# Performance work log

Hardware: AMD Instinct MI355X
Metric: run time of the kernel (lower is better)

## Reference

```python
import jax, jax.numpy as jnp
import numpy as np

N = 25600            # 64 graphs x 400 ROIs
F_IN = 400
H = 128
E = 512000           # 8000 edges per graph
B = 64
G = 8
OUT = 2
NPG = 400            # nodes per graph
EPG = E // B         # edges per graph
BN_EPS = 1e-5


def _xavier(k, shape):
    lim = float(np.sqrt(6.0 / (shape[0] + shape[1])))
    return jax.random.uniform(k, shape, jnp.float32, -lim, lim)


def setup_inputs() -> dict:
    key = jax.random.key(0)
    ks = jax.random.split(key, 16)
    inp = {}
    inp["x"] = jax.random.normal(ks[0], (N, F_IN), jnp.float32)
    # within-graph random edges: local index + graph offset
    src_l = jax.random.randint(ks[1], (E,), 0, NPG, jnp.int32)
    dst_l = jax.random.randint(ks[2], (E,), 0, NPG, jnp.int32)
    off = (jnp.arange(E, dtype=jnp.int32) // EPG) * NPG
    inp["edge_index"] = jnp.stack([src_l + off, dst_l + off])
    inp["batch"] = (jnp.arange(N, dtype=jnp.int32) // NPG)
    inp["group_ids"] = jax.random.randint(ks[3], (N,), 0, G, jnp.int32)
    inp["ge"] = _xavier(ks[4], (G, 2))
    inp["he"] = _xavier(ks[5], (2, 2))
    dims = [(F_IN + 4, H), (H, H), (H, H)]
    for i, (di, do) in enumerate(dims):
        k1, k2 = jax.random.split(ks[6 + i])
        inp[f"w{i}a"] = _xavier(k1, (di, do))
        inp[f"b{i}a"] = jnp.zeros((do,), jnp.float32)
        inp[f"g{i}"] = jnp.ones((do,), jnp.float32)
        inp[f"be{i}"] = jnp.zeros((do,), jnp.float32)
        inp[f"w{i}b"] = _xavier(k2, (do, do))
        inp[f"b{i}b"] = jnp.zeros((do,), jnp.float32)
    inp["wfa"] = _xavier(ks[10], (H, H))
    inp["bfa"] = jnp.zeros((H,), jnp.float32)
    inp["wfb"] = _xavier(ks[11], (H, OUT))
    inp["bfb"] = jnp.zeros((OUT,), jnp.float32)
    return inp


def _bn(h, gamma, beta):
    # BatchNorm1d in training mode: stats over node dimension
    mu = jnp.mean(h, axis=0, keepdims=True)
    var = jnp.var(h, axis=0, keepdims=True)
    return gamma * (h - mu) * jax.lax.rsqrt(var + BN_EPS) + beta


def reference(x, edge_index, batch, group_ids, ge, he,
              w0a, b0a, g0, be0, w0b, b0b,
              w1a, b1a, g1, be1, w1b, b1b,
              w2a, b2a, g2, be2, w2b, b2b,
              wfa, bfa, wfb, bfb):
    n = x.shape[0]
    hemi = jnp.arange(n) % 2                      # [1::2] = 1
    h = jnp.concatenate([x, ge[group_ids], he[hemi]], axis=-1)  # [N, F_IN+4]
    src, dst = edge_index[0], edge_index[1]
    layers = [(w0a, b0a, g0, be0, w0b, b0b),
              (w1a, b1a, g1, be1, w1b, b1b),
              (w2a, b2a, g2, be2, w2b, b2b)]
    for wa, ba, g, be, wb, bb in layers:
        # GINConv (eps=0): x_i + sum_{(j,i)} x_j, then 2-layer MLP w/ batchnorm
        agg = jax.ops.segment_sum(h[src], dst, num_segments=N)
        z = h + agg
        z = jax.nn.relu(_bn(z @ wa + ba, g, be))  # dropout = identity (eval)
        h = jax.nn.relu(z @ wb + bb)              # outer ReLU from forward()
    pooled = jax.ops.segment_sum(h, batch, num_segments=B)  # global_add_pool
    return jax.nn.relu(pooled @ wfa + bfa) @ wfb + bfb
```

## Files before the change

kernel.cpp:

```cpp
#include <hip/hip_runtime.h>

#define N_NODES 25600
#define F_IN 400
#define NE 512000
#define NB 64
#define NPG 400
#define EPG 8000
#define BN_EPS 1e-5f

#define S_ROWS 448
#define S_COLS 448
#define AGG_TILES 14
#define SB_RPB 112
#define K0PAD 448

typedef __attribute__((ext_vector_type(8))) short short8;
typedef __attribute__((ext_vector_type(4))) short short4_t;
typedef __attribute__((ext_vector_type(4))) float floatx4;

__device__ __forceinline__ unsigned short f2bf(float f) {
    unsigned int u = __float_as_uint(f);
    u += 0x7FFF + ((u >> 16) & 1);
    return (unsigned short)(u >> 16);
}
__device__ __forceinline__ float bf2f(unsigned short s) {
    return __uint_as_float((unsigned int)s << 16);
}
__device__ __forceinline__ short u8bf(unsigned v) {
    return (short)(__float_as_uint((float)v) >> 16);
}


__global__ __launch_bounds__(256) void prep(const int* __restrict__ src,
                                            const int* __restrict__ dst,
                                            unsigned char* __restrict__ Sb,
                                            const float* __restrict__ wa0, const float* __restrict__ wa1,
                                            const float* __restrict__ wa2, const float* __restrict__ wb0,
                                            const float* __restrict__ wb1, const float* __restrict__ wb2,
                                            unsigned short* __restrict__ t0, unsigned short* __restrict__ t1,
                                            unsigned short* __restrict__ t2, unsigned short* __restrict__ t3,
                                            unsigned short* __restrict__ t4, unsigned short* __restrict__ t5,
                                            float* __restrict__ pstat) {
    __shared__ int cnt32[SB_RPB * NPG / 4];
    int tid = threadIdx.x;
    if (blockIdx.x < 256) {
        int b = blockIdx.x;
        int g = b >> 2, part = b & 3;
        int r0 = part * SB_RPB;
        for (int i = tid; i < SB_RPB * NPG / 4; i += 256) cnt32[i] = 0;
        __syncthreads();
        int ebase = g * EPG, nbase = g * NPG;
        for (int e = tid; e < EPG; e += 256) {
            int d = dst[ebase + e] - nbase;
            int dr = d - r0;
            if ((unsigned)dr < (unsigned)SB_RPB) {
                int s = src[ebase + e] - nbase;
                int idx = dr * NPG + s;
                atomicAdd(&cnt32[idx >> 2], (int)(1u << ((idx & 3) * 8)));
            }
        }
        __syncthreads();
        const unsigned char* cb = (const unsigned char*)cnt32;
        for (int i = tid; i < SB_RPB * (S_COLS / 8); i += 256) {
            int rr = i / (S_COLS / 8), c8 = (i % (S_COLS / 8)) * 8;
            int R = r0 + rr;
            unsigned lo = 0, hi = 0;
#pragma unroll
            for (int j = 0; j < 4; ++j) {
                int c = c8 + j;
                unsigned v = 0;
                if (R < NPG && c < NPG) v = (unsigned)cb[rr * NPG + c] + (c == R ? 1u : 0u);
                lo |= v << (8 * j);
            }
#pragma unroll
            for (int j = 0; j < 4; ++j) {
                int c = c8 + 4 + j;
                unsigned v = 0;
                if (R < NPG && c < NPG) v = (unsigned)cb[rr * NPG + c] + (c == R ? 1u : 0u);
                hi |= v << (8 * j);
            }
            uint2 o = {lo, hi};
            *(uint2*)&Sb[((size_t)g * S_ROWS + R) * S_COLS + c8] = o;
        }
        return;
    }
    int idx = (blockIdx.x - 256) * 256 + tid;
    if (idx < 3 * 2048) pstat[idx] = 0.f;
    if (idx < 128 * K0PAD) {
        int n = idx / K0PAD, k = idx - n * K0PAD;
        t0[idx] = (k < 400) ? f2bf(wa0[(size_t)k * 128 + n]) : (unsigned short)0;
        return;
    }
    idx -= 128 * K0PAD;
    if (idx >= 5 * 128 * 128) return;
    int seg = idx >> 14;
    int r = idx & 16383;
    int n = r >> 7, k = r & 127;
    const float* srcs[5] = {wb0, wa1, wb1, wa2, wb2};
    unsigned short* dsts[5] = {t3, t1, t4, t2, t5};
    dsts[seg][r] = f2bf(srcs[seg][(size_t)k * 128 + n]);
}


__global__ __launch_bounds__(256) void gemm_embed32(const float* __restrict__ A,
                                                    const unsigned short* __restrict__ Wt,
                                                    const float* __restrict__ Wfull,
                                                    const int* __restrict__ gid,
                                                    const float* __restrict__ ge,
                                                    const float* __restrict__ he,
                                                    unsigned short* __restrict__ CtT) {
    __shared__ __align__(16) unsigned short As[32][72];
    __shared__ __align__(16) unsigned short Bs[128][72];
    __shared__ float Wex[4][128];
    int tid = threadIdx.x;
    int m0 = blockIdx.x * 32;
    int wave = tid >> 6, lane = tid & 63;
    int wcol = wave * 32;
    int fm = lane & 15, quad = lane >> 4;

    for (int i = tid; i < 512; i += 256)
        Wex[i >> 7][i & 127] = Wfull[(size_t)(400 + (i >> 7)) * 128 + (i & 127)];

    floatx4 acc[2][2];
#pragma unroll
    for (int rt = 0; rt < 2; ++rt)
#pragma unroll
        for (int ct = 0; ct < 2; ++ct) acc[rt][ct] = (floatx4){0.f, 0.f, 0.f, 0.f};

    const int rA = tid >> 3, kcA = (tid & 7) * 8;
    const int nB = tid >> 1, kcB = (tid & 1) * 32;
    float4 aP0, aP1;
    short8 bP0, bP1, bP2, bP3;

    auto loadK = [&](int ks) {
        int k0 = ks * 64;
        int kg = k0 + kcA;
        if (kg + 7 < 400) {
            const float* ar = A + (size_t)(m0 + rA) * F_IN + kg;
            aP0 = *(const float4*)ar;
            aP1 = *(const float4*)(ar + 4);
        } else {
            const float* ar = A + (size_t)(m0 + rA) * F_IN;
            float v[8];
#pragma unroll
            for (int j = 0; j < 8; ++j) v[j] = (kg + j < 400) ? ar[kg + j] : 0.f;
            aP0 = (float4){v[0], v[1], v[2], v[3]};
            aP1 = (float4){v[4], v[5], v[6], v[7]};
        }
        const unsigned short* wr = Wt + (size_t)nB * K0PAD + k0 + kcB;
        bP0 = *(const short8*)wr;
        bP1 = *(const short8*)(wr + 8);
        bP2 = *(const short8*)(wr + 16);
        bP3 = *(const short8*)(wr + 24);
    };

    loadK(0);
    for (int ks = 0; ks < 7; ++ks) {
        {
            short8 s;
            s[0] = (short)f2bf(aP0.x); s[1] = (short)f2bf(aP0.y);
            s[2] = (short)f2bf(aP0.z); s[3] = (short)f2bf(aP0.w);
            s[4] = (short)f2bf(aP1.x); s[5] = (short)f2bf(aP1.y);
            s[6] = (short)f2bf(aP1.z); s[7] = (short)f2bf(aP1.w);
            *(short8*)&As[rA][kcA] = s;
            *(short8*)&Bs[nB][kcB] = bP0;
            *(short8*)&Bs[nB][kcB + 8] = bP1;
            *(short8*)&Bs[nB][kcB + 16] = bP2;
            *(short8*)&Bs[nB][kcB + 24] = bP3;
        }
        __syncthreads();
        if (ks + 1 < 7) loadK(ks + 1);
#pragma unroll
        for (int k0l = 0; k0l < 64; k0l += 32) {
            short8 af[2], bf[2];
            af[0] = *(const short8*)&As[fm][k0l + quad * 8];
            af[1] = *(const short8*)&As[16 + fm][k0l + quad * 8];
#pragma unroll
            for (int ct = 0; ct < 2; ++ct)
                bf[ct] = *(const short8*)&Bs[wcol + ct * 16 + fm][k0l + quad * 8];
#pragma unroll
            for (int rt = 0; rt < 2; ++rt)
#pragma unroll
                for (int ct = 0; ct < 2; ++ct)
                    acc[rt][ct] = __builtin_amdgcn_mfma_f32_16x16x32_bf16(
                        af[rt], bf[ct], acc[rt][ct], 0, 0, 0);
        }
        __syncthreads();
    }

#pragma unroll
    for (int rt = 0; rt < 2; ++rt) {
#pragma unroll
        for (int ct = 0; ct < 2; ++ct) {
            int col = wcol + ct * 16 + fm;
            int row0 = m0 + rt * 16 + quad * 4;
            ushort4 o;
#pragma unroll
            for (int r = 0; r < 4; ++r) {
                int row = row0 + r;
                int gv = gid[row];
                float v = acc[rt][ct][r]
                        + ge[gv * 2] * Wex[0][col] + ge[gv * 2 + 1] * Wex[1][col]
                        + he[(row & 1) * 2] * Wex[2][col] + he[(row & 1) * 2 + 1] * Wex[3][col];
                ((unsigned short*)&o)[r] = f2bf(v);
            }
            *(ushort4*)&CtT[(size_t)col * N_NODES + row0] = o;
        }
    }
}


__global__ __launch_bounds__(256) void agg_mfma(const unsigned char* __restrict__ Sb,
                                                const unsigned short* __restrict__ tT,
                                                const float* __restrict__ bias,
                                                unsigned short* __restrict__ z,
                                                float* __restrict__ psumG,
                                                float* __restrict__ psqG) {
    __shared__ __align__(16) unsigned short As[32][72];
    __shared__ __align__(16) unsigned short Bs[128][72];
    __shared__ float sw[4][2][16], qw[4][2][16];
    int tid = threadIdx.x;
    int b = blockIdx.x;
    int g = b & 63;
    int tile = b >> 6;
    int m0l = tile * 32;
    int node0 = g * NPG;
    int wave = tid >> 6, lane = tid & 63;
    int wcol = wave * 32;
    int fm = lane & 15, quad = lane >> 4;

    floatx4 acc[2][2];
#pragma unroll
    for (int rt = 0; rt < 2; ++rt)
#pragma unroll
        for (int ct = 0; ct < 2; ++ct) acc[rt][ct] = (floatx4){0.f, 0.f, 0.f, 0.f};

    const int rA = tid >> 3, kcA = (tid & 7) * 8;
    const int nB = tid >> 1, kcB = (tid & 1) * 32;
    uint2 aP;
    short8 bP0, bP1, bP2, bP3;

    auto loadK = [&](int ks) {
        int k0 = ks * 64;
        aP = *(const uint2*)(Sb + ((size_t)g * S_ROWS + m0l + rA) * S_COLS + k0 + kcA);
        const unsigned short* p = tT + (size_t)nB * N_NODES + node0 + k0 + kcB;
        bP0 = *(const short8*)p;
        bP1 = *(const short8*)(p + 8);
        bP2 = *(const short8*)(p + 16);
        bP3 = *(const short8*)(p + 24);
    };

    loadK(0);
    for (int ks = 0; ks < S_COLS / 64; ++ks) {
        {
            short8 s;
#pragma unroll
            for (int j = 0; j < 4; ++j) s[j] = u8bf((aP.x >> (8 * j)) & 255u);
#pragma unroll
            for (int j = 0; j < 4; ++j) s[4 + j] = u8bf((aP.y >> (8 * j)) & 255u);
            *(short8*)&As[rA][kcA] = s;
            *(short8*)&Bs[nB][kcB] = bP0;
            *(short8*)&Bs[nB][kcB + 8] = bP1;
            *(short8*)&Bs[nB][kcB + 16] = bP2;
            *(short8*)&Bs[nB][kcB + 24] = bP3;
        }
        __syncthreads();
        if (ks + 1 < S_COLS / 64) loadK(ks + 1);
#pragma unroll
        for (int k0l = 0; k0l < 64; k0l += 32) {
            short8 af[2], bf[2];
            af[0] = *(const short8*)&As[fm][k0l + quad * 8];
            af[1] = *(const short8*)&As[16 + fm][k0l + quad * 8];
#pragma unroll
            for (int ct = 0; ct < 2; ++ct)
                bf[ct] = *(const short8*)&Bs[wcol + ct * 16 + fm][k0l + quad * 8];
#pragma unroll
            for (int rt = 0; rt < 2; ++rt)
#pragma unroll
                for (int ct = 0; ct < 2; ++ct)
                    acc[rt][ct] = __builtin_amdgcn_mfma_f32_16x16x32_bf16(
                        af[rt], bf[ct], acc[rt][ct], 0, 0, 0);
        }
        __syncthreads();
    }

    {
        float scol[2] = {0.f, 0.f}, qcol[2] = {0.f, 0.f};
#pragma unroll
        for (int rt = 0; rt < 2; ++rt) {
#pragma unroll
            for (int ct = 0; ct < 2; ++ct) {
                int col = wcol + ct * 16 + fm;
                float bv = bias[col];
                int rbase = m0l + rt * 16 + quad * 4;
#pragma unroll
                for (int r = 0; r < 4; ++r) {
                    int rloc = rbase + r;
                    if (rloc < NPG) {
                        float v = acc[rt][ct][r] + bv;
                        z[(size_t)(node0 + rloc) * 128 + col] = f2bf(v);
                        scol[ct] += v;
                        qcol[ct] += v * v;
                    }
                }
            }
        }
#pragma unroll
        for (int ct = 0; ct < 2; ++ct) {
            scol[ct] += __shfl_xor(scol[ct], 16);
            scol[ct] += __shfl_xor(scol[ct], 32);
            qcol[ct] += __shfl_xor(qcol[ct], 16);
            qcol[ct] += __shfl_xor(qcol[ct], 32);
        }
        if (lane < 16) {
#pragma unroll
            for (int ct = 0; ct < 2; ++ct) { sw[wave][ct][lane] = scol[ct]; qw[wave][ct][lane] = qcol[ct]; }
        }
    }
    __syncthreads();
    if (tid < 128) {
        int c = tid;
        int wv = c >> 5, ct = (c >> 4) & 1, f = c & 15;
        int bucket = b & 7;
        atomicAdd(&psumG[bucket * 128 + c], sw[wv][ct][f]);
        atomicAdd(&psqG[bucket * 128 + c], qw[wv][ct][f]);
    }
}


#define MODE_FUSED 0
#define MODE_FINAL 1

template <int MODE>
__global__ __launch_bounds__(256) void gemm_post32(const unsigned short* __restrict__ z,
                                                   const float* __restrict__ psumG,
                                                   const float* __restrict__ psqG,
                                                   const float* __restrict__ gamma,
                                                   const float* __restrict__ beta,
                                                   const unsigned short* __restrict__ wtb,
                                                   const float* __restrict__ bb,
                                                   const unsigned short* __restrict__ wta_next,
                                                   unsigned short* __restrict__ CtT,
                                                   unsigned short* __restrict__ Hout) {
    __shared__ __align__(16) unsigned short As[32][72];
    __shared__ __align__(16) unsigned short Bs[128][72];
    __shared__ __align__(16) unsigned short hs[32][136];
    __shared__ float coefs[256];
    int tid = threadIdx.x;
    int m0 = blockIdx.x * 32;
    int wave = tid >> 6, lane = tid & 63;
    int wcol = wave * 32;
    int fm = lane & 15, quad = lane >> 4;

    if (tid < 128) {
        float S = 0.f, Q = 0.f;
#pragma unroll
        for (int b = 0; b < 8; ++b) { S += psumG[b * 128 + tid]; Q += psqG[b * 128 + tid]; }
        float invn = 1.0f / (float)N_NODES;
        float mu = S * invn;
        float var = Q * invn - mu * mu;
        float a = gamma[tid] * rsqrtf(var + BN_EPS);
        coefs[tid] = a;
        coefs[128 + tid] = beta[tid] - a * mu;
    }
    __syncthreads();

    floatx4 acc[2][2];
#pragma unroll
    for (int rt = 0; rt < 2; ++rt)
#pragma unroll
        for (int ct = 0; ct < 2; ++ct) acc[rt][ct] = (floatx4){0.f, 0.f, 0.f, 0.f};

    const int rA = tid >> 3, kcA = (tid & 7) * 8;
    const int nB = tid >> 1, kcB = (tid & 1) * 32;
    short8 aP;
    short8 bP0, bP1, bP2, bP3;

    auto loadK1 = [&](int ks) {
        int k0 = ks * 64;
        aP = *(const short8*)&z[(size_t)(m0 + rA) * 128 + k0 + kcA];
        const unsigned short* wr = wtb + (size_t)nB * 128 + k0 + kcB;
        bP0 = *(const short8*)wr;
        bP1 = *(const short8*)(wr + 8);
        bP2 = *(const short8*)(wr + 16);
        bP3 = *(const short8*)(wr + 24);
    };

    loadK1(0);
    for (int ks = 0; ks < 2; ++ks) {
        {
            int kg = ks * 64 + kcA;
            short8 s;
#pragma unroll
            for (int j = 0; j < 8; ++j) {
                float v = fmaxf(coefs[kg + j] * bf2f((unsigned short)aP[j]) + coefs[128 + kg + j], 0.f);
                s[j] = (short)f2bf(v);
            }
            *(short8*)&As[rA][kcA] = s;
            *(short8*)&Bs[nB][kcB] = bP0;
            *(short8*)&Bs[nB][kcB + 8] = bP1;
            *(short8*)&Bs[nB][kcB + 16] = bP2;
            *(short8*)&Bs[nB][kcB + 24] = bP3;
        }
        __syncthreads();
        if (ks + 1 < 2) loadK1(ks + 1);
#pragma unroll
        for (int k0l = 0; k0l < 64; k0l += 32) {
            short8 af[2], bf[2];
            af[0] = *(const short8*)&As[fm][k0l + quad * 8];
            af[1] = *(const short8*)&As[16 + fm][k0l + quad * 8];
#pragma unroll
            for (int ct = 0; ct < 2; ++ct)
                bf[ct] = *(const short8*)&Bs[wcol + ct * 16 + fm][k0l + quad * 8];
#pragma unroll
            for (int rt = 0; rt < 2; ++rt)
#pragma unroll
                for (int ct = 0; ct < 2; ++ct)
                    acc[rt][ct] = __builtin_amdgcn_mfma_f32_16x16x32_bf16(
                        af[rt], bf[ct], acc[rt][ct], 0, 0, 0);
        }
        __syncthreads();
    }

    if (MODE == MODE_FINAL) {
#pragma unroll
        for (int rt = 0; rt < 2; ++rt)
#pragma unroll
            for (int ct = 0; ct < 2; ++ct) {
                int col = wcol + ct * 16 + fm;
                float bv = bb[col];
                int rbase = m0 + rt * 16 + quad * 4;
#pragma unroll
                for (int r = 0; r < 4; ++r)
                    Hout[(size_t)(rbase + r) * 128 + col] = f2bf(fmaxf(acc[rt][ct][r] + bv, 0.f));
            }
        return;
    }

#pragma unroll
    for (int rt = 0; rt < 2; ++rt)
#pragma unroll
        for (int ct = 0; ct < 2; ++ct) {
            int col = wcol + ct * 16 + fm;
            float bv = bb[col];
            int rbase = rt * 16 + quad * 4;
#pragma unroll
            for (int r = 0; r < 4; ++r)
                hs[rbase + r][col] = f2bf(fmaxf(acc[rt][ct][r] + bv, 0.f));
        }
    __syncthreads();

#pragma unroll
    for (int rt = 0; rt < 2; ++rt)
#pragma unroll
        for (int ct = 0; ct < 2; ++ct) acc[rt][ct] = (floatx4){0.f, 0.f, 0.f, 0.f};

    const int kcB2 = (tid & 1) * 16;
    for (int ks = 0; ks < 4; ++ks) {
        int k0 = ks * 32;
        {
            const unsigned short* wr = wta_next + (size_t)nB * 128 + k0 + kcB2;
            *(short8*)&Bs[nB][kcB2] = *(const short8*)wr;
            *(short8*)&Bs[nB][kcB2 + 8] = *(const short8*)(wr + 8);
        }
        __syncthreads();
        {
            short8 af[2], bf[2];
            af[0] = *(const short8*)&hs[fm][k0 + quad * 8];
            af[1] = *(const short8*)&hs[16 + fm][k0 + quad * 8];
#pragma unroll
            for (int ct = 0; ct < 2; ++ct)
                bf[ct] = *(const short8*)&Bs[wcol + ct * 16 + fm][kcB2 - kcB2 + quad * 8];
#pragma unroll
            for (int rt = 0; rt < 2; ++rt)
#pragma unroll
                for (int ct = 0; ct < 2; ++ct)
                    acc[rt][ct] = __builtin_amdgcn_mfma_f32_16x16x32_bf16(
                        af[rt], bf[ct], acc[rt][ct], 0, 0, 0);
        }
        __syncthreads();
    }

#pragma unroll
    for (int rt = 0; rt < 2; ++rt)
#pragma unroll
        for (int ct = 0; ct < 2; ++ct) {
            int col = wcol + ct * 16 + fm;
            int row0 = m0 + rt * 16 + quad * 4;
            ushort4 o;
#pragma unroll
            for (int r = 0; r < 4; ++r) ((unsigned short*)&o)[r] = f2bf(acc[rt][ct][r]);
            *(ushort4*)&CtT[(size_t)col * N_NODES + row0] = o;
        }
}


__global__ __launch_bounds__(128) void head(const unsigned short* __restrict__ h,
                                            const float* __restrict__ wfa,
                                            const float* __restrict__ bfa,
                                            const float* __restrict__ wfb,
                                            const float* __restrict__ bfb,
                                            float* __restrict__ out) {
    int g = blockIdx.x;
    int f = threadIdx.x;
    const unsigned short* hg = h + (size_t)g * NPG * 128;
    float pooled = 0.f;
    for (int n = 0; n < NPG; n += 4) {
        pooled += bf2f(hg[(n + 0) * 128 + f]);
        pooled += bf2f(hg[(n + 1) * 128 + f]);
        pooled += bf2f(hg[(n + 2) * 128 + f]);
        pooled += bf2f(hg[(n + 3) * 128 + f]);
    }
    __shared__ float pl[128];
    pl[f] = pooled;
    __syncthreads();
    float a = bfa[f];
    for (int k = 0; k < 128; ++k) a += pl[k] * wfa[k * 128 + f];
    float p2 = fmaxf(a, 0.f);
    __shared__ float o0[128], o1[128];
    o0[f] = p2 * wfb[f * 2 + 0];
    o1[f] = p2 * wfb[f * 2 + 1];
    __syncthreads();
    if (f == 0) {
        float a0 = bfb[0], a1 = bfb[1];
#pragma unroll
        for (int k = 0; k < 128; ++k) { a0 += o0[k]; a1 += o1[k]; }
        out[g * 2 + 0] = a0;
        out[g * 2 + 1] = a1;
    }
}


extern "C" void kernel_launch(void* const* d_in, const int* in_sizes, int n_in,
                              void* d_out, int out_size, void* d_ws, size_t ws_size,
                              hipStream_t stream) {
    const float* x   = (const float*)d_in[0];
    const int* ei    = (const int*)d_in[1];
    const int* gid   = (const int*)d_in[3];
    const float* ge  = (const float*)d_in[4];
    const float* he  = (const float*)d_in[5];
    const float* wa[3] = {(const float*)d_in[6],  (const float*)d_in[12], (const float*)d_in[18]};
    const float* ba[3] = {(const float*)d_in[7],  (const float*)d_in[13], (const float*)d_in[19]};
    const float* gg[3] = {(const float*)d_in[8],  (const float*)d_in[14], (const float*)d_in[20]};
    const float* bb_[3]= {(const float*)d_in[9],  (const float*)d_in[15], (const float*)d_in[21]};
    const float* wb[3] = {(const float*)d_in[10], (const float*)d_in[16], (const float*)d_in[22]};
    const float* bbias[3] = {(const float*)d_in[11], (const float*)d_in[17], (const float*)d_in[23]};
    const float* wfa = (const float*)d_in[24];
    const float* bfa = (const float*)d_in[25];
    const float* wfb = (const float*)d_in[26];
    const float* bfb = (const float*)d_in[27];
    float* out = (float*)d_out;

    char* ws = (char*)d_ws;
    size_t o = 0;
    auto alloc = [&](size_t bytes) { char* p = ws + o; o += (bytes + 255) & ~(size_t)255; return p; };
    unsigned short* tT = (unsigned short*)alloc((size_t)128 * N_NODES * 2 + 1024);
    unsigned short* z  = (unsigned short*)alloc((size_t)N_NODES * 128 * 2);
    unsigned short* h  = (unsigned short*)alloc((size_t)N_NODES * 128 * 2);
    unsigned char* Sb  = (unsigned char*)alloc((size_t)NB * S_ROWS * S_COLS);
    float* pstat = (float*)alloc(3 * 2048 * 4);
    unsigned short* wt0  = (unsigned short*)alloc(128 * K0PAD * 2);
    unsigned short* wta1 = (unsigned short*)alloc(128 * 128 * 2);
    unsigned short* wta2 = (unsigned short*)alloc(128 * 128 * 2);
    unsigned short* wtb0 = (unsigned short*)alloc(128 * 128 * 2);
    unsigned short* wtb1 = (unsigned short*)alloc(128 * 128 * 2);
    unsigned short* wtb2 = (unsigned short*)alloc(128 * 128 * 2);
    (void)ws_size; (void)in_sizes; (void)n_in; (void)out_size;

    const int* esrc_in = ei;
    const int* edst_in = ei + NE;

    prep<<<256 + 544, 256, 0, stream>>>(esrc_in, edst_in, Sb,
                                        wa[0], wa[1], wa[2], wb[0], wb[1], wb[2],
                                        wt0, wta1, wta2, wtb0, wtb1, wtb2, pstat);

    float* ps0 = pstat;            float* pq0 = pstat + 1024;
    float* ps1 = pstat + 2048;     float* pq1 = pstat + 3072;
    float* ps2 = pstat + 4096;     float* pq2 = pstat + 5120;

    gemm_embed32<<<800, 256, 0, stream>>>(x, wt0, wa[0], gid, ge, he, tT);
    agg_mfma<<<NB * AGG_TILES, 256, 0, stream>>>(Sb, tT, ba[0], z, ps0, pq0);
    gemm_post32<MODE_FUSED><<<800, 256, 0, stream>>>(z, ps0, pq0, gg[0], bb_[0],
                                                     wtb0, bbias[0], wta1, tT, nullptr);
    agg_mfma<<<NB * AGG_TILES, 256, 0, stream>>>(Sb, tT, ba[1], z, ps1, pq1);
    gemm_post32<MODE_FUSED><<<800, 256, 0, stream>>>(z, ps1, pq1, gg[1], bb_[1],
                                                     wtb1, bbias[1], wta2, tT, nullptr);
    agg_mfma<<<NB * AGG_TILES, 256, 0, stream>>>(Sb, tT, ba[2], z, ps2, pq2);
    gemm_post32<MODE_FINAL><<<800, 256, 0, stream>>>(z, ps2, pq2, gg[2], bb_[2],
                                                     wtb2, bbias[2], nullptr, nullptr, h);

    head<<<NB, 128, 0, stream>>>(h, wfa, bfa, wfb, bfb, out);
}
```

Baseline: 265.4 us.

## Pack adjacency counts to 4-bit and fuse global pooling into final layer

Stores per-graph edge count matrix as 4-bit nibbles instead of bytes, halving the adjacency traffic read by each aggregation GEMM. The last post-GEMM kernel now reduces its ReLU outputs per graph and atomically accumulates them into a pooled buffer, removing the write of the full hidden matrix and the head kernel's serial scan over it. Risks: counts above 15 would silently wrap, and atomics add contention and nondeterministic summation order.

```diff
diff --git a/kernel.cpp b/kernel.cpp
--- a/kernel.cpp
+++ b/kernel.cpp
@@ -10,6 +10,7 @@
 
 #define S_ROWS 448
 #define S_COLS 448
+#define S_COLS2 (S_COLS / 2)
 #define AGG_TILES 14
 #define SB_RPB 112
 #define K0PAD 448
@@ -64,28 +65,20 @@
         for (int i = tid; i < SB_RPB * (S_COLS / 8); i += 256) {
             int rr = i / (S_COLS / 8), c8 = (i % (S_COLS / 8)) * 8;
             int R = r0 + rr;
-            unsigned lo = 0, hi = 0;
-#pragma unroll
-            for (int j = 0; j < 4; ++j) {
+            unsigned pk = 0;
+#pragma unroll
+            for (int j = 0; j < 8; ++j) {
                 int c = c8 + j;
                 unsigned v = 0;
                 if (R < NPG && c < NPG) v = (unsigned)cb[rr * NPG + c] + (c == R ? 1u : 0u);
-                lo |= v << (8 * j);
-            }
-#pragma unroll
-            for (int j = 0; j < 4; ++j) {
-                int c = c8 + 4 + j;
-                unsigned v = 0;
-                if (R < NPG && c < NPG) v = (unsigned)cb[rr * NPG + c] + (c == R ? 1u : 0u);
-                hi |= v << (8 * j);
-            }
-            uint2 o = {lo, hi};
-            *(uint2*)&Sb[((size_t)g * S_ROWS + R) * S_COLS + c8] = o;
+                pk |= (v & 15u) << (4 * j);
+            }
+            *(unsigned*)&Sb[((size_t)g * S_ROWS + R) * S_COLS2 + (c8 >> 1)] = pk;
         }
         return;
     }
     int idx = (blockIdx.x - 256) * 256 + tid;
-    if (idx < 3 * 2048) pstat[idx] = 0.f;
+    if (idx < 3 * 2048 + 8192) pstat[idx] = 0.f;
     if (idx < 128 * K0PAD) {
         int n = idx / K0PAD, k = idx - n * K0PAD;
         t0[idx] = (k < 400) ? f2bf(wa0[(size_t)k * 128 + n]) : (unsigned short)0;
@@ -237,12 +230,12 @@
 
     const int rA = tid >> 3, kcA = (tid & 7) * 8;
     const int nB = tid >> 1, kcB = (tid & 1) * 32;
-    uint2 aP;
+    unsigned aP;
     short8 bP0, bP1, bP2, bP3;
 
     auto loadK = [&](int ks) {
         int k0 = ks * 64;
-        aP = *(const uint2*)(Sb + ((size_t)g * S_ROWS + m0l + rA) * S_COLS + k0 + kcA);
+        aP = *(const unsigned*)(Sb + ((size_t)g * S_ROWS + m0l + rA) * S_COLS2 + ((k0 + kcA) >> 1));
         const unsigned short* p = tT + (size_t)nB * N_NODES + node0 + k0 + kcB;
         bP0 = *(const short8*)p;
         bP1 = *(const short8*)(p + 8);
@@ -255,9 +248,7 @@
         {
             short8 s;
 #pragma unroll
-            for (int j = 0; j < 4; ++j) s[j] = u8bf((aP.x >> (8 * j)) & 255u);
-#pragma unroll
-            for (int j = 0; j < 4; ++j) s[4 + j] = u8bf((aP.y >> (8 * j)) & 255u);
+            for (int j = 0; j < 8; ++j) s[j] = u8bf((aP >> (4 * j)) & 15u);
             *(short8*)&As[rA][kcA] = s;
             *(short8*)&Bs[nB][kcB] = bP0;
             *(short8*)&Bs[nB][kcB + 8] = bP1;
@@ -341,7 +332,7 @@
                                                    const float* __restrict__ bb,
                                                    const unsigned short* __restrict__ wta_next,
                                                    unsigned short* __restrict__ CtT,
-                                                   unsigned short* __restrict__ Hout) {
+                                                   float* __restrict__ pooled) {
     __shared__ __align__(16) unsigned short As[32][72];
     __shared__ __align__(16) unsigned short Bs[128][72];
     __shared__ __align__(16) unsigned short hs[32][136];
@@ -423,17 +414,37 @@
     }
 
     if (MODE == MODE_FINAL) {
+        float rsum[2][2];
 #pragma unroll
         for (int rt = 0; rt < 2; ++rt)
 #pragma unroll
             for (int ct = 0; ct < 2; ++ct) {
                 int col = wcol + ct * 16 + fm;
                 float bv = bb[col];
-                int rbase = m0 + rt * 16 + quad * 4;
-#pragma unroll
-                for (int r = 0; r < 4; ++r)
-                    Hout[(size_t)(rbase + r) * 128 + col] = f2bf(fmaxf(acc[rt][ct][r] + bv, 0.f));
-            }
+                float s = 0.f;
+#pragma unroll
+                for (int r = 0; r < 4; ++r) s += fmaxf(acc[rt][ct][r] + bv, 0.f);
+                rsum[rt][ct] = s;
+            }
+        bool uniform = (m0 / NPG) == ((m0 + 31) / NPG);
+        if (uniform) {
+            int gph = m0 / NPG;
+#pragma unroll
+            for (int ct = 0; ct < 2; ++ct) {
+                float cs = rsum[0][ct] + rsum[1][ct];
+                cs += __shfl_xor(cs, 16);
+                cs += __shfl_xor(cs, 32);
+                if (lane < 16) atomicAdd(&pooled[gph * 128 + wcol + ct * 16 + fm], cs);
+            }
+        } else {
+#pragma unroll
+            for (int rt = 0; rt < 2; ++rt)
+#pragma unroll
+                for (int ct = 0; ct < 2; ++ct) {
+                    int gph = (m0 + rt * 16 + quad * 4) / NPG;
+                    atomicAdd(&pooled[gph * 128 + wcol + ct * 16 + fm], rsum[rt][ct]);
+                }
+        }
         return;
     }
 
@@ -470,7 +481,7 @@
             af[1] = *(const short8*)&hs[16 + fm][k0 + quad * 8];
 #pragma unroll
             for (int ct = 0; ct < 2; ++ct)
-                bf[ct] = *(const short8*)&Bs[wcol + ct * 16 + fm][kcB2 - kcB2 + quad * 8];
+                bf[ct] = *(const short8*)&Bs[wcol + ct * 16 + fm][quad * 8];
 #pragma unroll
             for (int rt = 0; rt < 2; ++rt)
 #pragma unroll
@@ -495,7 +506,7 @@
 }
 
 
-__global__ __launch_bounds__(128) void head(const unsigned short* __restrict__ h,
+__global__ __launch_bounds__(128) void head(const float* __restrict__ pooled,
                                             const float* __restrict__ wfa,
                                             const float* __restrict__ bfa,
                                             const float* __restrict__ wfb,
@@ -503,16 +514,8 @@
                                             float* __restrict__ out) {
     int g = blockIdx.x;
     int f = threadIdx.x;
-    const unsigned short* hg = h + (size_t)g * NPG * 128;
-    float pooled = 0.f;
-    for (int n = 0; n < NPG; n += 4) {
-        pooled += bf2f(hg[(n + 0) * 128 + f]);
-        pooled += bf2f(hg[(n + 1) * 128 + f]);
-        pooled += bf2f(hg[(n + 2) * 128 + f]);
-        pooled += bf2f(hg[(n + 3) * 128 + f]);
-    }
     __shared__ float pl[128];
-    pl[f] = pooled;
+    pl[f] = pooled[g * 128 + f];
     __syncthreads();
     float a = bfa[f];
     for (int k = 0; k < 128; ++k) a += pl[k] * wfa[k * 128 + f];
@@ -556,9 +559,8 @@
     auto alloc = [&](size_t bytes) { char* p = ws + o; o += (bytes + 255) & ~(size_t)255; return p; };
     unsigned short* tT = (unsigned short*)alloc((size_t)128 * N_NODES * 2 + 1024);
     unsigned short* z  = (unsigned short*)alloc((size_t)N_NODES * 128 * 2);
-    unsigned short* h  = (unsigned short*)alloc((size_t)N_NODES * 128 * 2);
-    unsigned char* Sb  = (unsigned char*)alloc((size_t)NB * S_ROWS * S_COLS);
-    float* pstat = (float*)alloc(3 * 2048 * 4);
+    unsigned char* Sb  = (unsigned char*)alloc((size_t)NB * S_ROWS * S_COLS2);
+    float* pstat = (float*)alloc((3 * 2048 + 8192) * 4);
     unsigned short* wt0  = (unsigned short*)alloc(128 * K0PAD * 2);
     unsigned short* wta1 = (unsigned short*)alloc(128 * 128 * 2);
     unsigned short* wta2 = (unsigned short*)alloc(128 * 128 * 2);
@@ -577,6 +579,7 @@
     float* ps0 = pstat;            float* pq0 = pstat + 1024;
     float* ps1 = pstat + 2048;     float* pq1 = pstat + 3072;
     float* ps2 = pstat + 4096;     float* pq2 = pstat + 5120;
+    float* pooled = pstat + 6144;
 
     gemm_embed32<<<800, 256, 0, stream>>>(x, wt0, wa[0], gid, ge, he, tT);
     agg_mfma<<<NB * AGG_TILES, 256, 0, stream>>>(Sb, tT, ba[0], z, ps0, pq0);
@@ -587,7 +590,7 @@
                                                      wtb1, bbias[1], wta2, tT, nullptr);
     agg_mfma<<<NB * AGG_TILES, 256, 0, stream>>>(Sb, tT, ba[2], z, ps2, pq2);
     gemm_post32<MODE_FINAL><<<800, 256, 0, stream>>>(z, ps2, pq2, gg[2], bb_[2],
-                                                     wtb2, bbias[2], nullptr, nullptr, h);
-
-    head<<<NB, 128, 0, stream>>>(h, wfa, bfa, wfb, bfb, out);
-}
+                                                     wtb2, bbias[2], nullptr, nullptr, pooled);
+
+    head<<<NB, 128, 0, stream>>>(pooled, wfa, bfa, wfb, bfb, out);
+}
```

Measured after the change: 254.7 us. -4.1%, faster.
